# Kernel tuning notes

Measured on AMD Instinct MI355X. Metric: run time of the kernel, lower is better.

## Reference

```python
import jax, jax.numpy as jnp
import numpy as np

B, T, C, NH = 4, 2048, 1024, 16
HS = C // NH


def setup_inputs() -> dict:
    key = jax.random.key(0)
    k1, k2, k3, k4, k5 = jax.random.split(key, 5)
    s = 1.0 / np.sqrt(C)
    return {
        "x": jax.random.normal(k1, (B, T, C), dtype=jnp.float32),
        "Wqkv": jax.random.normal(k2, (3 * C, C), dtype=jnp.float32) * s,
        "bqkv": jax.random.normal(k3, (3 * C,), dtype=jnp.float32) * 0.02,
        "Wproj": jax.random.normal(k4, (C, C), dtype=jnp.float32) * s,
        "bproj": jax.random.normal(k5, (C,), dtype=jnp.float32) * 0.02,
    }


def reference(x, Wqkv, bqkv, Wproj, bproj):
    Bsz, Tlen, Cdim = x.shape
    # qkv projection (torch Linear: x @ W.T + b)
    qkv = x @ Wqkv.T + bqkv                      # [B, T, 3C]
    q, k, v = jnp.split(qkv, 3, axis=-1)
    # [B, NH, T, HS]
    q = q.reshape(Bsz, Tlen, NH, HS).transpose(0, 2, 1, 3)
    k = k.reshape(Bsz, Tlen, NH, HS).transpose(0, 2, 1, 3)
    v = v.reshape(Bsz, Tlen, NH, HS).transpose(0, 2, 1, 3)
    scale = 1.0 / np.sqrt(HS)
    att = jnp.einsum('bhqd,bhkd->bhqk', q, k) * scale
    causal = jnp.triu(jnp.ones((Tlen, Tlen), dtype=bool), k=1)
    att = jnp.where(causal[None, None], -jnp.inf, att)
    att = jax.nn.softmax(att, axis=-1)
    y = jnp.einsum('bhqk,bhkd->bhqd', att, v)    # [B, NH, T, HS]
    y = y.transpose(0, 2, 1, 3).reshape(Bsz, Tlen, Cdim)
    return y @ Wproj.T + bproj
```

## Files before the change

### kernel.cpp

```cpp
#include <hip/hip_runtime.h>
#include <hip/hip_bf16.h>

#define B_   4
#define T_   2048
#define C_   1024
#define NH_  16
#define HS_  64
#define M_   8192
#define N1_  3072
#define BH_  64

typedef __attribute__((ext_vector_type(8))) short short8;
typedef __attribute__((ext_vector_type(4))) short short4v;
typedef __attribute__((ext_vector_type(4))) float f32x4;

__device__ __forceinline__ short f2bf(float f) {
  unsigned u = __float_as_uint(f);
  unsigned r = (u + 0x7fffu + ((u >> 16) & 1u)) >> 16;
  return (short)r;
}
__device__ __forceinline__ unsigned pk_bf16(float a, float b) {
  __hip_bfloat162 h = __float22bfloat162_rn(make_float2(a, b));
  union { __hip_bfloat162 h2; unsigned u; } cv; cv.h2 = h; return cv.u;
}

typedef __attribute__((address_space(1))) unsigned int as1_uint;
typedef __attribute__((address_space(3))) unsigned int as3_uint;
__device__ __forceinline__ void g2l16(const void* g, void* l) {
  __builtin_amdgcn_global_load_lds((as1_uint*)g, (as3_uint*)l, 16, 0, 0);
}

__global__ __launch_bounds__(256) void conv_bf16(
    const float* __restrict__ src, short* __restrict__ dst)
{
  const size_t i = ((size_t)blockIdx.x * 256 + threadIdx.x) * 8;
  const f32x4 a = *(const f32x4*)&src[i];
  const f32x4 b = *(const f32x4*)&src[i + 4];
  short8 o;
  o[0] = f2bf(a[0]); o[1] = f2bf(a[1]); o[2] = f2bf(a[2]); o[3] = f2bf(a[3]);
  o[4] = f2bf(b[0]); o[5] = f2bf(b[1]); o[6] = f2bf(b[2]); o[7] = f2bf(b[3]);
  *(short8*)&dst[i] = o;
}

__global__ __launch_bounds__(256) void qkv_gemm(
    const short* __restrict__ X,
    const short* __restrict__ W,
    const float* __restrict__ bias,
    short* __restrict__ Qo, short* __restrict__ Ko, short* __restrict__ Vt)
{
  __shared__ short As[128 * 32];
  __shared__ short Bs[128 * 32];
  const int tid = threadIdx.x;
  const int lane = tid & 63;
  const int wid = tid >> 6;
  const int wy = wid >> 1, wx = wid & 1;
  const int lq = lane >> 4, lm = lane & 15;
  const int row0 = blockIdx.x * 128;
  const int col0 = blockIdx.y * 128;

  f32x4 acc[4][4] = {};

  const int c0 = tid, c1 = tid + 256;
  const int ar0 = c0 >> 2, ak0 = (c0 & 3) << 3;
  const int ar1 = c1 >> 2, ak1 = (c1 & 3) << 3;

  for (int k0 = 0; k0 < C_; k0 += 32) {
    __syncthreads();
    g2l16(&X[(size_t)(row0 + ar0) * C_ + k0 + ak0], &As[c0 * 8]);
    g2l16(&X[(size_t)(row0 + ar1) * C_ + k0 + ak1], &As[c1 * 8]);
    g2l16(&W[(size_t)(col0 + ar0) * C_ + k0 + ak0], &Bs[c0 * 8]);
    g2l16(&W[(size_t)(col0 + ar1) * C_ + k0 + ak1], &Bs[c1 * 8]);
    __syncthreads();

    short8 af[4], bfr[4];
#pragma unroll
    for (int mi = 0; mi < 4; ++mi)
      af[mi] = *(const short8*)&As[(wy * 64 + mi * 16 + lm) * 32 + lq * 8];
#pragma unroll
    for (int ni = 0; ni < 4; ++ni)
      bfr[ni] = *(const short8*)&Bs[(wx * 64 + ni * 16 + lm) * 32 + lq * 8];
#pragma unroll
    for (int mi = 0; mi < 4; ++mi)
#pragma unroll
      for (int ni = 0; ni < 4; ++ni)
        acc[mi][ni] = __builtin_amdgcn_mfma_f32_16x16x32_bf16(af[mi], bfr[ni], acc[mi][ni], 0, 0, 0);
  }

#pragma unroll
  for (int ni = 0; ni < 4; ++ni) {
    const int n = col0 + wx * 64 + ni * 16 + lm;
    const float bv = bias[n];
    const int sel = n >> 10;
    const int cc = n & (C_ - 1);
    const int h = cc >> 6, d = cc & 63;
    if (sel == 2) {
#pragma unroll
      for (int mi = 0; mi < 4; ++mi) {
        const int m0 = row0 + wy * 64 + mi * 16 + lq * 4;
        const int b = m0 >> 11, t0 = m0 & (T_ - 1);
        const int bh = b * NH_ + h;
        short4v o;
#pragma unroll
        for (int i = 0; i < 4; ++i) o[i] = f2bf(acc[mi][ni][i] + bv);
        *(short4v*)&Vt[((size_t)bh * HS_ + d) * T_ + t0] = o;
      }
    } else {
      short* dst = (sel == 0) ? Qo : Ko;
#pragma unroll
      for (int mi = 0; mi < 4; ++mi) {
#pragma unroll
        for (int i = 0; i < 4; ++i) {
          const int m = row0 + wy * 64 + mi * 16 + lq * 4 + i;
          const int b = m >> 11, t = m & (T_ - 1);
          const int bh = b * NH_ + h;
          dst[((size_t)bh * T_ + t) * HS_ + d] = f2bf(acc[mi][ni][i] + bv);
        }
      }
    }
  }
}

__global__ __launch_bounds__(256) void proj_gemm(
    const short* __restrict__ Y,
    const short* __restrict__ W,
    const float* __restrict__ bias,
    float* __restrict__ Out)
{
  __shared__ short As[128 * 32];
  __shared__ short Bs[128 * 32];
  const int tid = threadIdx.x;
  const int lane = tid & 63;
  const int wid = tid >> 6;
  const int wy = wid >> 1, wx = wid & 1;
  const int lq = lane >> 4, lm = lane & 15;
  const int row0 = blockIdx.x * 128;
  const int col0 = blockIdx.y * 128;

  f32x4 acc[4][4] = {};

  const int c0 = tid, c1 = tid + 256;
  const int ar0 = c0 >> 2, ak0 = (c0 & 3) << 3;
  const int ar1 = c1 >> 2, ak1 = (c1 & 3) << 3;

  for (int k0 = 0; k0 < C_; k0 += 32) {
    __syncthreads();
    g2l16(&Y[(size_t)(row0 + ar0) * C_ + k0 + ak0], &As[c0 * 8]);
    g2l16(&Y[(size_t)(row0 + ar1) * C_ + k0 + ak1], &As[c1 * 8]);
    g2l16(&W[(size_t)(col0 + ar0) * C_ + k0 + ak0], &Bs[c0 * 8]);
    g2l16(&W[(size_t)(col0 + ar1) * C_ + k0 + ak1], &Bs[c1 * 8]);
    __syncthreads();

    short8 af[4], bfr[4];
#pragma unroll
    for (int mi = 0; mi < 4; ++mi)
      af[mi] = *(const short8*)&As[(wy * 64 + mi * 16 + lm) * 32 + lq * 8];
#pragma unroll
    for (int ni = 0; ni < 4; ++ni)
      bfr[ni] = *(const short8*)&Bs[(wx * 64 + ni * 16 + lm) * 32 + lq * 8];
#pragma unroll
    for (int mi = 0; mi < 4; ++mi)
#pragma unroll
      for (int ni = 0; ni < 4; ++ni)
        acc[mi][ni] = __builtin_amdgcn_mfma_f32_16x16x32_bf16(af[mi], bfr[ni], acc[mi][ni], 0, 0, 0);
  }

#pragma unroll
  for (int ni = 0; ni < 4; ++ni) {
    const int n = col0 + wx * 64 + ni * 16 + lm;
    const float bv = bias[n];
#pragma unroll
    for (int mi = 0; mi < 4; ++mi) {
#pragma unroll
      for (int i = 0; i < 4; ++i) {
        const int m = row0 + wy * 64 + mi * 16 + lq * 4 + i;
        Out[(size_t)m * C_ + n] = acc[mi][ni][i] + bv;
      }
    }
  }
}

#define LDK 72
__global__ __launch_bounds__(256) void attn(
    const short* __restrict__ Qg, const short* __restrict__ Kg,
    const short* __restrict__ Vg, short* __restrict__ Yo)
{
  __shared__ short Ks[64 * LDK];
  __shared__ short Vs[64 * LDK];

  const int tid = threadIdx.x;
  const int lane = tid & 63;
  const int w = tid >> 6;
  const int lq = lane >> 4, lm = lane & 15;
  const int bh = blockIdx.y;
  const int b = bh >> 4, h = bh & 15;
  const size_t base = (size_t)bh * T_ * HS_;
  const short* __restrict__ Kb = Kg + base;
  const short* __restrict__ Vb = Vg + base;
  const float sf = 0.125f * 1.44269504089f;

  const int sr = tid >> 3;
  const int sc = (tid & 7) * 8;

#pragma unroll 1
  for (int half = 0; half < 2; ++half) {
    const int qt = half ? (int)blockIdx.x : 31 - (int)blockIdx.x;
    const int q0 = qt * 64;
    const int q = q0 + w * 16 + lm;

    const short8 qf0 = *(const short8*)&Qg[base + (size_t)q * HS_ + lq * 8];
    const short8 qf1 = *(const short8*)&Qg[base + (size_t)q * HS_ + 32 + lq * 8];

    float m_run = -3.0e38f, l_run = 0.0f;
    f32x4 o_acc[4] = {};

    short8 pk0 = *(const short8*)&Kb[(size_t)sr * HS_ + sc];
    short8 pk1 = *(const short8*)&Kb[(size_t)(32 + sr) * HS_ + sc];
    short8 pv0 = *(const short8*)&Vb[(size_t)sr * T_ + sc];
    short8 pv1 = *(const short8*)&Vb[(size_t)(32 + sr) * T_ + sc];

#pragma unroll 1
    for (int kt = 0; kt <= qt; ++kt) {
      const int kv0 = kt * 64;

      __syncthreads();
      *(short8*)&Ks[sr * LDK + sc] = pk0;
      *(short8*)&Ks[(32 + sr) * LDK + sc] = pk1;
      *(short8*)&Vs[sr * LDK + sc] = pv0;
      *(short8*)&Vs[(32 + sr) * LDK + sc] = pv1;
      __syncthreads();

      if (kt < qt) {
        const int nk = kv0 + 64;
        pk0 = *(const short8*)&Kb[(size_t)(nk + sr) * HS_ + sc];
        pk1 = *(const short8*)&Kb[(size_t)(nk + 32 + sr) * HS_ + sc];
        pv0 = *(const short8*)&Vb[(size_t)sr * T_ + nk + sc];
        pv1 = *(const short8*)&Vb[(size_t)(32 + sr) * T_ + nk + sc];
      }

      f32x4 sv[4];
#pragma unroll
      for (int ni = 0; ni < 4; ++ni) {
        const short8 kf0 = *(const short8*)&Ks[(ni * 16 + lm) * LDK + lq * 8];
        const short8 kf1 = *(const short8*)&Ks[(ni * 16 + lm) * LDK + 32 + lq * 8];
        f32x4 s = {};
        s = __builtin_amdgcn_mfma_f32_16x16x32_bf16(kf0, qf0, s, 0, 0, 0);
        sv[ni] = __builtin_amdgcn_mfma_f32_16x16x32_bf16(kf1, qf1, s, 0, 0, 0);
      }

      if (kt == qt) {
#pragma unroll
        for (int ni = 0; ni < 4; ++ni) {
          const int kvb = kv0 + ni * 16 + lq * 4;
#pragma unroll
          for (int i = 0; i < 4; ++i)
            if (kvb + i > q) sv[ni][i] = -3.0e38f;
        }
      }

      float v = fmaxf(fmaxf(fmaxf(sv[0][0], sv[0][1]), fmaxf(sv[0][2], sv[0][3])),
                      fmaxf(fmaxf(sv[1][0], sv[1][1]), fmaxf(sv[1][2], sv[1][3])));
      v = fmaxf(v, fmaxf(fmaxf(fmaxf(sv[2][0], sv[2][1]), fmaxf(sv[2][2], sv[2][3])),
                         fmaxf(fmaxf(sv[3][0], sv[3][1]), fmaxf(sv[3][2], sv[3][3]))));
      v = fmaxf(v, __shfl_xor(v, 16));
      v = fmaxf(v, __shfl_xor(v, 32));
      const float mnew = fmaxf(m_run, v);
      const float alpha = __builtin_amdgcn_exp2f((m_run - mnew) * sf);
      const float nb = -mnew * sf;
      m_run = mnew;

#pragma unroll
      for (int ni = 0; ni < 4; ++ni)
#pragma unroll
        for (int i = 0; i < 4; ++i)
          sv[ni][i] = __builtin_amdgcn_exp2f(__builtin_fmaf(sv[ni][i], sf, nb));

      float s = ((sv[0][0] + sv[0][1]) + (sv[0][2] + sv[0][3]))
              + ((sv[1][0] + sv[1][1]) + (sv[1][2] + sv[1][3]))
              + ((sv[2][0] + sv[2][1]) + (sv[2][2] + sv[2][3]))
              + ((sv[3][0] + sv[3][1]) + (sv[3][2] + sv[3][3]));
      s += __shfl_xor(s, 16);
      s += __shfl_xor(s, 32);
      l_run = l_run * alpha + s;

#pragma unroll
      for (int di = 0; di < 4; ++di)
#pragma unroll
        for (int i = 0; i < 4; ++i)
          o_acc[di][i] *= alpha;

      short4v p4[4];
#pragma unroll
      for (int ni = 0; ni < 4; ++ni) {
        union { short4v s4; unsigned u[2]; } pk;
        pk.u[0] = pk_bf16(sv[ni][0], sv[ni][1]);
        pk.u[1] = pk_bf16(sv[ni][2], sv[ni][3]);
        p4[ni] = pk.s4;
      }

#pragma unroll
      for (int di = 0; di < 4; ++di) {
#pragma unroll
        for (int ni = 0; ni < 4; ++ni) {
          const short4v vfr = *(const short4v*)&Vs[(di * 16 + lm) * LDK + ni * 16 + lq * 4];
          o_acc[di] = __builtin_amdgcn_mfma_f32_16x16x16bf16_1k(vfr, p4[ni], o_acc[di], 0, 0, 0);
        }
      }
    }

    const float rl = 1.0f / l_run;
    const size_t rowo = ((size_t)(b * T_ + q)) * C_ + h * HS_;
#pragma unroll
    for (int di = 0; di < 4; ++di) {
      union { short4v s4; unsigned u[2]; } pk;
      pk.u[0] = pk_bf16(o_acc[di][0] * rl, o_acc[di][1] * rl);
      pk.u[1] = pk_bf16(o_acc[di][2] * rl, o_acc[di][3] * rl);
      *(short4v*)&Yo[rowo + di * 16 + lq * 4] = pk.s4;
    }
  }
}

extern "C" void kernel_launch(void* const* d_in, const int* in_sizes, int n_in,
                              void* d_out, int out_size, void* d_ws, size_t ws_size,
                              hipStream_t stream) {
  (void)in_sizes; (void)n_in; (void)out_size;
  const float* x     = (const float*)d_in[0];
  const float* Wqkv  = (const float*)d_in[1];
  const float* bqkv  = (const float*)d_in[2];
  const float* Wproj = (const float*)d_in[3];
  const float* bproj = (const float*)d_in[4];
  float* out = (float*)d_out;

  const size_t nWq = (size_t)N1_ * C_;
  const size_t nWp = (size_t)C_ * C_;
  const size_t nFull = (size_t)M_ * C_;
  const size_t nB = (size_t)T_ * C_;

  dim3 blk(256);
  const size_t need_batched = (nWq + nWp + 4 * nFull) * sizeof(short);

  if (ws_size >= need_batched) {
    short* Wq_bf = (short*)d_ws;
    short* Wp_bf = Wq_bf + nWq;
    short* S0    = Wp_bf + nWp;
    short* Qw    = S0 + nFull;
    short* Kw    = Qw + nFull;
    short* Vw    = Kw + nFull;

    conv_bf16<<<dim3((int)(nWq / 2048)), blk, 0, stream>>>(Wqkv, Wq_bf);
    conv_bf16<<<dim3((int)(nWp / 2048)), blk, 0, stream>>>(Wproj, Wp_bf);
    conv_bf16<<<dim3((int)(nFull / 2048)), blk, 0, stream>>>(x, S0);
    qkv_gemm<<<dim3(M_ / 128, N1_ / 128), blk, 0, stream>>>(S0, Wq_bf, bqkv, Qw, Kw, Vw);
    attn<<<dim3(16, BH_), blk, 0, stream>>>(Qw, Kw, Vw, S0);
    proj_gemm<<<dim3(M_ / 128, C_ / 128), blk, 0, stream>>>(S0, Wp_bf, bproj, out);
  } else {
    short* Wq_bf = (short*)d_ws;
    short* Wp_bf = Wq_bf + nWq;
    short* S0    = Wp_bf + nWp;
    short* Qw    = S0 + nB;
    short* Kw    = Qw + nB;
    short* Vw    = Kw + nB;

    conv_bf16<<<dim3((int)(nWq / 2048)), blk, 0, stream>>>(Wqkv, Wq_bf);
    conv_bf16<<<dim3((int)(nWp / 2048)), blk, 0, stream>>>(Wproj, Wp_bf);
    for (int b = 0; b < B_; ++b) {
      const float* xb = x   + (size_t)b * nB;
      float*       ob = out + (size_t)b * nB;
      conv_bf16<<<dim3((int)(nB / 2048)), blk, 0, stream>>>(xb, S0);
      qkv_gemm<<<dim3(T_ / 128, N1_ / 128), blk, 0, stream>>>(S0, Wq_bf, bqkv, Qw, Kw, Vw);
      attn<<<dim3(16, NH_), blk, 0, stream>>>(Qw, Kw, Vw, S0);
      proj_gemm<<<dim3(T_ / 128, C_ / 128), blk, 0, stream>>>(S0, Wp_bf, bproj, ob);
    }
  }
}
```

Baseline: 290.8 us.

## Widen GEMM K-tile, split attention to one q-tile per block, lazy rescale

Both GEMMs now stage 64-wide K slices per barrier pair instead of 32, halving the number of syncs and doubling LDS use per block. The attention kernel no longer pairs two query tiles per block; it launches 32 blocks per head, each handling one tile, which removes the serial half loop but leaves load balance across blocks to the scheduler. It also adds a thresholded lazy softmax rescale that skips the alpha update when the max grows by less than 8 in log2 units, and raises wave priority around the MFMA sections. The lazy rescale lets exponentials reach up to 2^8, which slightly changes numeric behavior in bf16.

New measurement: 340.2 us. +17.0%, slower.

```diff
diff --git a/kernel.cpp b/kernel.cpp
--- a/kernel.cpp
+++ b/kernel.cpp
@@ -48,8 +48,8 @@
     const float* __restrict__ bias,
     short* __restrict__ Qo, short* __restrict__ Ko, short* __restrict__ Vt)
 {
-  __shared__ short As[128 * 32];
-  __shared__ short Bs[128 * 32];
+  __shared__ short As[128 * 64];
+  __shared__ short Bs[128 * 64];
   const int tid = threadIdx.x;
   const int lane = tid & 63;
   const int wid = tid >> 6;
@@ -60,30 +60,34 @@
 
   f32x4 acc[4][4] = {};
 
-  const int c0 = tid, c1 = tid + 256;
-  const int ar0 = c0 >> 2, ak0 = (c0 & 3) << 3;
-  const int ar1 = c1 >> 2, ak1 = (c1 & 3) << 3;
-
-  for (int k0 = 0; k0 < C_; k0 += 32) {
-    __syncthreads();
-    g2l16(&X[(size_t)(row0 + ar0) * C_ + k0 + ak0], &As[c0 * 8]);
-    g2l16(&X[(size_t)(row0 + ar1) * C_ + k0 + ak1], &As[c1 * 8]);
-    g2l16(&W[(size_t)(col0 + ar0) * C_ + k0 + ak0], &Bs[c0 * 8]);
-    g2l16(&W[(size_t)(col0 + ar1) * C_ + k0 + ak1], &Bs[c1 * 8]);
-    __syncthreads();
-
-    short8 af[4], bfr[4];
-#pragma unroll
-    for (int mi = 0; mi < 4; ++mi)
-      af[mi] = *(const short8*)&As[(wy * 64 + mi * 16 + lm) * 32 + lq * 8];
-#pragma unroll
-    for (int ni = 0; ni < 4; ++ni)
-      bfr[ni] = *(const short8*)&Bs[(wx * 64 + ni * 16 + lm) * 32 + lq * 8];
-#pragma unroll
-    for (int mi = 0; mi < 4; ++mi)
+  const int ar = tid >> 3;
+  const int ac = (tid & 7) << 3;
+
+  for (int k0 = 0; k0 < C_; k0 += 64) {
+    __syncthreads();
+#pragma unroll
+    for (int j = 0; j < 4; ++j) {
+      const int r = ar + j * 32;
+      g2l16(&X[(size_t)(row0 + r) * C_ + k0 + ac], &As[r * 64 + ac]);
+      g2l16(&W[(size_t)(col0 + r) * C_ + k0 + ac], &Bs[r * 64 + ac]);
+    }
+    __syncthreads();
+
+#pragma unroll
+    for (int kk = 0; kk < 2; ++kk) {
+      short8 af[4], bfr[4];
+#pragma unroll
+      for (int mi = 0; mi < 4; ++mi)
+        af[mi] = *(const short8*)&As[(wy * 64 + mi * 16 + lm) * 64 + kk * 32 + lq * 8];
 #pragma unroll
       for (int ni = 0; ni < 4; ++ni)
-        acc[mi][ni] = __builtin_amdgcn_mfma_f32_16x16x32_bf16(af[mi], bfr[ni], acc[mi][ni], 0, 0, 0);
+        bfr[ni] = *(const short8*)&Bs[(wx * 64 + ni * 16 + lm) * 64 + kk * 32 + lq * 8];
+#pragma unroll
+      for (int mi = 0; mi < 4; ++mi)
+#pragma unroll
+        for (int ni = 0; ni < 4; ++ni)
+          acc[mi][ni] = __builtin_amdgcn_mfma_f32_16x16x32_bf16(af[mi], bfr[ni], acc[mi][ni], 0, 0, 0);
+    }
   }
 
 #pragma unroll
@@ -126,8 +130,8 @@
     const float* __restrict__ bias,
     float* __restrict__ Out)
 {
-  __shared__ short As[128 * 32];
-  __shared__ short Bs[128 * 32];
+  __shared__ short As[128 * 64];
+  __shared__ short Bs[128 * 64];
   const int tid = threadIdx.x;
   const int lane = tid & 63;
   const int wid = tid >> 6;
@@ -138,30 +142,34 @@
 
   f32x4 acc[4][4] = {};
 
-  const int c0 = tid, c1 = tid + 256;
-  const int ar0 = c0 >> 2, ak0 = (c0 & 3) << 3;
-  const int ar1 = c1 >> 2, ak1 = (c1 & 3) << 3;
-
-  for (int k0 = 0; k0 < C_; k0 += 32) {
-    __syncthreads();
-    g2l16(&Y[(size_t)(row0 + ar0) * C_ + k0 + ak0], &As[c0 * 8]);
-    g2l16(&Y[(size_t)(row0 + ar1) * C_ + k0 + ak1], &As[c1 * 8]);
-    g2l16(&W[(size_t)(col0 + ar0) * C_ + k0 + ak0], &Bs[c0 * 8]);
-    g2l16(&W[(size_t)(col0 + ar1) * C_ + k0 + ak1], &Bs[c1 * 8]);
-    __syncthreads();
-
-    short8 af[4], bfr[4];
-#pragma unroll
-    for (int mi = 0; mi < 4; ++mi)
-      af[mi] = *(const short8*)&As[(wy * 64 + mi * 16 + lm) * 32 + lq * 8];
-#pragma unroll
-    for (int ni = 0; ni < 4; ++ni)
-      bfr[ni] = *(const short8*)&Bs[(wx * 64 + ni * 16 + lm) * 32 + lq * 8];
-#pragma unroll
-    for (int mi = 0; mi < 4; ++mi)
+  const int ar = tid >> 3;
+  const int ac = (tid & 7) << 3;
+
+  for (int k0 = 0; k0 < C_; k0 += 64) {
+    __syncthreads();
+#pragma unroll
+    for (int j = 0; j < 4; ++j) {
+      const int r = ar + j * 32;
+      g2l16(&Y[(size_t)(row0 + r) * C_ + k0 + ac], &As[r * 64 + ac]);
+      g2l16(&W[(size_t)(col0 + r) * C_ + k0 + ac], &Bs[r * 64 + ac]);
+    }
+    __syncthreads();
+
+#pragma unroll
+    for (int kk = 0; kk < 2; ++kk) {
+      short8 af[4], bfr[4];
+#pragma unroll
+      for (int mi = 0; mi < 4; ++mi)
+        af[mi] = *(const short8*)&As[(wy * 64 + mi * 16 + lm) * 64 + kk * 32 + lq * 8];
 #pragma unroll
       for (int ni = 0; ni < 4; ++ni)
-        acc[mi][ni] = __builtin_amdgcn_mfma_f32_16x16x32_bf16(af[mi], bfr[ni], acc[mi][ni], 0, 0, 0);
+        bfr[ni] = *(const short8*)&Bs[(wx * 64 + ni * 16 + lm) * 64 + kk * 32 + lq * 8];
+#pragma unroll
+      for (int mi = 0; mi < 4; ++mi)
+#pragma unroll
+        for (int ni = 0; ni < 4; ++ni)
+          acc[mi][ni] = __builtin_amdgcn_mfma_f32_16x16x32_bf16(af[mi], bfr[ni], acc[mi][ni], 0, 0, 0);
+    }
   }
 
 #pragma unroll
@@ -201,121 +209,125 @@
   const int sr = tid >> 3;
   const int sc = (tid & 7) * 8;
 
+  const int qt = 31 - (int)blockIdx.x;
+  const int q0 = qt * 64;
+  const int q = q0 + w * 16 + lm;
+
+  const short8 qf0 = *(const short8*)&Qg[base + (size_t)q * HS_ + lq * 8];
+  const short8 qf1 = *(const short8*)&Qg[base + (size_t)q * HS_ + 32 + lq * 8];
+
+  float m_run = -3.0e38f, l_run = 0.0f;
+  f32x4 o_acc[4] = {};
+
+  short8 pk0 = *(const short8*)&Kb[(size_t)sr * HS_ + sc];
+  short8 pk1 = *(const short8*)&Kb[(size_t)(32 + sr) * HS_ + sc];
+  short8 pv0 = *(const short8*)&Vb[(size_t)sr * T_ + sc];
+  short8 pv1 = *(const short8*)&Vb[(size_t)(32 + sr) * T_ + sc];
+
 #pragma unroll 1
-  for (int half = 0; half < 2; ++half) {
-    const int qt = half ? (int)blockIdx.x : 31 - (int)blockIdx.x;
-    const int q0 = qt * 64;
-    const int q = q0 + w * 16 + lm;
-
-    const short8 qf0 = *(const short8*)&Qg[base + (size_t)q * HS_ + lq * 8];
-    const short8 qf1 = *(const short8*)&Qg[base + (size_t)q * HS_ + 32 + lq * 8];
-
-    float m_run = -3.0e38f, l_run = 0.0f;
-    f32x4 o_acc[4] = {};
-
-    short8 pk0 = *(const short8*)&Kb[(size_t)sr * HS_ + sc];
-    short8 pk1 = *(const short8*)&Kb[(size_t)(32 + sr) * HS_ + sc];
-    short8 pv0 = *(const short8*)&Vb[(size_t)sr * T_ + sc];
-    short8 pv1 = *(const short8*)&Vb[(size_t)(32 + sr) * T_ + sc];
-
-#pragma unroll 1
-    for (int kt = 0; kt <= qt; ++kt) {
-      const int kv0 = kt * 64;
-
-      __syncthreads();
-      *(short8*)&Ks[sr * LDK + sc] = pk0;
-      *(short8*)&Ks[(32 + sr) * LDK + sc] = pk1;
-      *(short8*)&Vs[sr * LDK + sc] = pv0;
-      *(short8*)&Vs[(32 + sr) * LDK + sc] = pv1;
-      __syncthreads();
-
-      if (kt < qt) {
-        const int nk = kv0 + 64;
-        pk0 = *(const short8*)&Kb[(size_t)(nk + sr) * HS_ + sc];
-        pk1 = *(const short8*)&Kb[(size_t)(nk + 32 + sr) * HS_ + sc];
-        pv0 = *(const short8*)&Vb[(size_t)sr * T_ + nk + sc];
-        pv1 = *(const short8*)&Vb[(size_t)(32 + sr) * T_ + nk + sc];
-      }
-
-      f32x4 sv[4];
+  for (int kt = 0; kt <= qt; ++kt) {
+    const int kv0 = kt * 64;
+
+    __syncthreads();
+    *(short8*)&Ks[sr * LDK + sc] = pk0;
+    *(short8*)&Ks[(32 + sr) * LDK + sc] = pk1;
+    *(short8*)&Vs[sr * LDK + sc] = pv0;
+    *(short8*)&Vs[(32 + sr) * LDK + sc] = pv1;
+    __syncthreads();
+
+    if (kt < qt) {
+      const int nk = kv0 + 64;
+      pk0 = *(const short8*)&Kb[(size_t)(nk + sr) * HS_ + sc];
+      pk1 = *(const short8*)&Kb[(size_t)(nk + 32 + sr) * HS_ + sc];
+      pv0 = *(const short8*)&Vb[(size_t)sr * T_ + nk + sc];
+      pv1 = *(const short8*)&Vb[(size_t)(32 + sr) * T_ + nk + sc];
+    }
+
+    f32x4 sv[4];
+    __builtin_amdgcn_s_setprio(1);
+#pragma unroll
+    for (int ni = 0; ni < 4; ++ni) {
+      const short8 kf0 = *(const short8*)&Ks[(ni * 16 + lm) * LDK + lq * 8];
+      const short8 kf1 = *(const short8*)&Ks[(ni * 16 + lm) * LDK + 32 + lq * 8];
+      f32x4 s = {};
+      s = __builtin_amdgcn_mfma_f32_16x16x32_bf16(kf0, qf0, s, 0, 0, 0);
+      sv[ni] = __builtin_amdgcn_mfma_f32_16x16x32_bf16(kf1, qf1, s, 0, 0, 0);
+    }
+    __builtin_amdgcn_s_setprio(0);
+
+    if (kt == qt) {
 #pragma unroll
       for (int ni = 0; ni < 4; ++ni) {
-        const short8 kf0 = *(const short8*)&Ks[(ni * 16 + lm) * LDK + lq * 8];
-        const short8 kf1 = *(const short8*)&Ks[(ni * 16 + lm) * LDK + 32 + lq * 8];
-        f32x4 s = {};
-        s = __builtin_amdgcn_mfma_f32_16x16x32_bf16(kf0, qf0, s, 0, 0, 0);
-        sv[ni] = __builtin_amdgcn_mfma_f32_16x16x32_bf16(kf1, qf1, s, 0, 0, 0);
-      }
-
-      if (kt == qt) {
-#pragma unroll
-        for (int ni = 0; ni < 4; ++ni) {
-          const int kvb = kv0 + ni * 16 + lq * 4;
-#pragma unroll
-          for (int i = 0; i < 4; ++i)
-            if (kvb + i > q) sv[ni][i] = -3.0e38f;
-        }
-      }
-
-      float v = fmaxf(fmaxf(fmaxf(sv[0][0], sv[0][1]), fmaxf(sv[0][2], sv[0][3])),
-                      fmaxf(fmaxf(sv[1][0], sv[1][1]), fmaxf(sv[1][2], sv[1][3])));
-      v = fmaxf(v, fmaxf(fmaxf(fmaxf(sv[2][0], sv[2][1]), fmaxf(sv[2][2], sv[2][3])),
-                         fmaxf(fmaxf(sv[3][0], sv[3][1]), fmaxf(sv[3][2], sv[3][3]))));
-      v = fmaxf(v, __shfl_xor(v, 16));
-      v = fmaxf(v, __shfl_xor(v, 32));
+        const int kvb = kv0 + ni * 16 + lq * 4;
+#pragma unroll
+        for (int i = 0; i < 4; ++i)
+          if (kvb + i > q) sv[ni][i] = -3.0e38f;
+      }
+    }
+
+    float v = fmaxf(fmaxf(fmaxf(sv[0][0], sv[0][1]), fmaxf(sv[0][2], sv[0][3])),
+                    fmaxf(fmaxf(sv[1][0], sv[1][1]), fmaxf(sv[1][2], sv[1][3])));
+    v = fmaxf(v, fmaxf(fmaxf(fmaxf(sv[2][0], sv[2][1]), fmaxf(sv[2][2], sv[2][3])),
+                       fmaxf(fmaxf(sv[3][0], sv[3][1]), fmaxf(sv[3][2], sv[3][3]))));
+    v = fmaxf(v, __shfl_xor(v, 16));
+    v = fmaxf(v, __shfl_xor(v, 32));
+
+    if (!__all((v - m_run) * sf <= 8.0f)) {
       const float mnew = fmaxf(m_run, v);
       const float alpha = __builtin_amdgcn_exp2f((m_run - mnew) * sf);
-      const float nb = -mnew * sf;
       m_run = mnew;
-
-#pragma unroll
-      for (int ni = 0; ni < 4; ++ni)
-#pragma unroll
-        for (int i = 0; i < 4; ++i)
-          sv[ni][i] = __builtin_amdgcn_exp2f(__builtin_fmaf(sv[ni][i], sf, nb));
-
-      float s = ((sv[0][0] + sv[0][1]) + (sv[0][2] + sv[0][3]))
-              + ((sv[1][0] + sv[1][1]) + (sv[1][2] + sv[1][3]))
-              + ((sv[2][0] + sv[2][1]) + (sv[2][2] + sv[2][3]))
-              + ((sv[3][0] + sv[3][1]) + (sv[3][2] + sv[3][3]));
-      s += __shfl_xor(s, 16);
-      s += __shfl_xor(s, 32);
-      l_run = l_run * alpha + s;
-
+      l_run *= alpha;
 #pragma unroll
       for (int di = 0; di < 4; ++di)
 #pragma unroll
         for (int i = 0; i < 4; ++i)
           o_acc[di][i] *= alpha;
-
-      short4v p4[4];
+    }
+    const float nb = -m_run * sf;
+
+#pragma unroll
+    for (int ni = 0; ni < 4; ++ni)
+#pragma unroll
+      for (int i = 0; i < 4; ++i)
+        sv[ni][i] = __builtin_amdgcn_exp2f(__builtin_fmaf(sv[ni][i], sf, nb));
+
+    float s = ((sv[0][0] + sv[0][1]) + (sv[0][2] + sv[0][3]))
+            + ((sv[1][0] + sv[1][1]) + (sv[1][2] + sv[1][3]))
+            + ((sv[2][0] + sv[2][1]) + (sv[2][2] + sv[2][3]))
+            + ((sv[3][0] + sv[3][1]) + (sv[3][2] + sv[3][3]));
+    s += __shfl_xor(s, 16);
+    s += __shfl_xor(s, 32);
+    l_run += s;
+
+    short4v p4[4];
+#pragma unroll
+    for (int ni = 0; ni < 4; ++ni) {
+      union { short4v s4; unsigned u[2]; } pk;
+      pk.u[0] = pk_bf16(sv[ni][0], sv[ni][1]);
+      pk.u[1] = pk_bf16(sv[ni][2], sv[ni][3]);
+      p4[ni] = pk.s4;
+    }
+
+    __builtin_amdgcn_s_setprio(1);
+#pragma unroll
+    for (int di = 0; di < 4; ++di) {
 #pragma unroll
       for (int ni = 0; ni < 4; ++ni) {
-        union { short4v s4; unsigned u[2]; } pk;
-        pk.u[0] = pk_bf16(sv[ni][0], sv[ni][1]);
-        pk.u[1] = pk_bf16(sv[ni][2], sv[ni][3]);
-        p4[ni] = pk.s4;
-      }
-
-#pragma unroll
-      for (int di = 0; di < 4; ++di) {
-#pragma unroll
-        for (int ni = 0; ni < 4; ++ni) {
-          const short4v vfr = *(const short4v*)&Vs[(di * 16 + lm) * LDK + ni * 16 + lq * 4];
-          o_acc[di] = __builtin_amdgcn_mfma_f32_16x16x16bf16_1k(vfr, p4[ni], o_acc[di], 0, 0, 0);
-        }
-      }
-    }
-
-    const float rl = 1.0f / l_run;
-    const size_t rowo = ((size_t)(b * T_ + q)) * C_ + h * HS_;
-#pragma unroll
-    for (int di = 0; di < 4; ++di) {
-      union { short4v s4; unsigned u[2]; } pk;
-      pk.u[0] = pk_bf16(o_acc[di][0] * rl, o_acc[di][1] * rl);
-      pk.u[1] = pk_bf16(o_acc[di][2] * rl, o_acc[di][3] * rl);
-      *(short4v*)&Yo[rowo + di * 16 + lq * 4] = pk.s4;
-    }
+        const short4v vfr = *(const short4v*)&Vs[(di * 16 + lm) * LDK + ni * 16 + lq * 4];
+        o_acc[di] = __builtin_amdgcn_mfma_f32_16x16x16bf16_1k(vfr, p4[ni], o_acc[di], 0, 0, 0);
+      }
+    }
+    __builtin_amdgcn_s_setprio(0);
+  }
+
+  const float rl = 1.0f / l_run;
+  const size_t rowo = ((size_t)(b * T_ + q)) * C_ + h * HS_;
+#pragma unroll
+  for (int di = 0; di < 4; ++di) {
+    union { short4v s4; unsigned u[2]; } pk;
+    pk.u[0] = pk_bf16(o_acc[di][0] * rl, o_acc[di][1] * rl);
+    pk.u[1] = pk_bf16(o_acc[di][2] * rl, o_acc[di][3] * rl);
+    *(short4v*)&Yo[rowo + di * 16 + lq * 4] = pk.s4;
   }
 }
 
@@ -350,7 +362,7 @@
     conv_bf16<<<dim3((int)(nWp / 2048)), blk, 0, stream>>>(Wproj, Wp_bf);
     conv_bf16<<<dim3((int)(nFull / 2048)), blk, 0, stream>>>(x, S0);
     qkv_gemm<<<dim3(M_ / 128, N1_ / 128), blk, 0, stream>>>(S0, Wq_bf, bqkv, Qw, Kw, Vw);
-    attn<<<dim3(16, BH_), blk, 0, stream>>>(Qw, Kw, Vw, S0);
+    attn<<<dim3(32, BH_), blk, 0, stream>>>(Qw, Kw, Vw, S0);
     proj_gemm<<<dim3(M_ / 128, C_ / 128), blk, 0, stream>>>(S0, Wp_bf, bproj, out);
   } else {
     short* Wq_bf = (short*)d_ws;
@@ -367,7 +379,7 @@
       float*       ob = out + (size_t)b * nB;
       conv_bf16<<<dim3((int)(nB / 2048)), blk, 0, stream>>>(xb, S0);
       qkv_gemm<<<dim3(T_ / 128, N1_ / 128), blk, 0, stream>>>(S0, Wq_bf, bqkv, Qw, Kw, Vw);
-      attn<<<dim3(16, NH_), blk, 0, stream>>>(Qw, Kw, Vw, S0);
+      attn<<<dim3(32, NH_), blk, 0, stream>>>(Qw, Kw, Vw, S0);
       proj_gemm<<<dim3(T_ / 128, C_ / 128), blk, 0, stream>>>(S0, Wp_bf, bproj, ob);
     }
   }
```
